# Kernel tuning notes

Measured on AMD Instinct MI355X. Metric: run time of the kernel, lower is better.

## Reference

```python
import jax, jax.numpy as jnp
import numpy as np

BATCH = 4096
FEATURES = 64
VOCAB = 580000
EMB_DIM = 32
MODELS = 512
SEQ_LEN = 128


def _positional_encoding(position, d_model):
    # Faithful to the numpy get_angles: 1/10000^(2*(i//2)/d_model), sin on even, cos on odd.
    pos = jnp.arange(position, dtype=jnp.float32)[:, None]          # [P, 1]
    i = jnp.arange(d_model, dtype=jnp.float32)[None, :]             # [1, D]
    angle_rates = 1.0 / jnp.power(10000.0, (2.0 * jnp.floor(i / 2.0)) / jnp.float32(d_model))
    angles = pos * angle_rates                                      # [P, D]
    even = (jnp.arange(d_model) % 2 == 0)[None, :]
    pe = jnp.where(even, jnp.sin(angles), jnp.cos(angles))
    return pe[None]                                                 # [1, P, D]


def setup_inputs() -> dict:
    key = jax.random.key(0)
    k1, k2, k3 = jax.random.split(key, 3)
    tokens = jax.random.randint(k1, (BATCH, FEATURES), 0, VOCAB, dtype=jnp.int32)
    emb_table = jax.random.normal(k2, (VOCAB, EMB_DIM), dtype=jnp.float32)
    W = jax.random.normal(k3, (FEATURES * EMB_DIM, MODELS), dtype=jnp.float32) * 0.02
    b = jnp.zeros((MODELS,), dtype=jnp.float32)
    return {"tokens": tokens, "emb_table": emb_table, "W": W, "b": b}


def reference(tokens, emb_table, W, b):
    B, F = tokens.shape
    # gather + scale by sqrt(models)
    x = emb_table[tokens] * jnp.sqrt(jnp.float32(MODELS))           # [B, F, E]
    x = x.reshape(B, F * EMB_DIM)                                   # [B, F*E]
    x = x @ W + b                                                   # [B, M]
    # tf.tile(row, [seq_len]) then reshape (seq_len, models) == broadcast over seq axis
    pe = _positional_encoding(SEQ_LEN, MODELS)                      # [1, S, M]
    out = x[:, None, :] + pe[:, :SEQ_LEN, :]                        # [B, S, M]
    return out
```

## Files before the change

### kernel.cpp

```cpp
#include <hip/hip_runtime.h>
#include <math.h>

#define BATCH   4096
#define FEAT    64
#define EMB     32
#define MODELS  512
#define SEQ     128
#define KDIM    (FEAT * EMB)

#define SQRT_MODELS 22.62741699796952f
#define LN10000     9.210340371976184f

typedef __attribute__((ext_vector_type(4))) float        f32x4;
typedef __attribute__((ext_vector_type(8))) short        bf16x8;
typedef __attribute__((ext_vector_type(4))) unsigned int u32x4;

#define WT_BYTES  ((size_t)MODELS * KDIM * 2)
#define PE_BYTES  ((size_t)SEQ * MODELS * 4)
#define X_BYTES   ((size_t)BATCH * MODELS * 4)
#define ABF_BYTES ((size_t)BATCH * KDIM * 2)
#define WS_MID    (WT_BYTES + PE_BYTES + X_BYTES)
#define WS_FULL   (WT_BYTES + PE_BYTES + X_BYTES + ABF_BYTES)

__device__ inline unsigned short bf16_rne(float f) {
    unsigned int b = __builtin_bit_cast(unsigned int, f);
    return (unsigned short)((b + 0x7FFFu + ((b >> 16) & 1u)) >> 16);
}

#define CVT_PK4(pk, v0, v1)                                                     \
    {                                                                           \
        unsigned int q0, q1, q2, q3;                                            \
        asm("v_cvt_pk_bf16_f32 %0, %1, %2" : "=v"(q0) : "v"(v0.x), "v"(v0.y));  \
        asm("v_cvt_pk_bf16_f32 %0, %1, %2" : "=v"(q1) : "v"(v0.z), "v"(v0.w));  \
        asm("v_cvt_pk_bf16_f32 %0, %1, %2" : "=v"(q2) : "v"(v1.x), "v"(v1.y));  \
        asm("v_cvt_pk_bf16_f32 %0, %1, %2" : "=v"(q3) : "v"(v1.z), "v"(v1.w));  \
        pk = (u32x4){q0, q1, q2, q3};                                           \
    }

__global__ __launch_bounds__(256)
void prep_all(const int* __restrict__ tokens, const float* __restrict__ emb,
              const float* __restrict__ W, const float* __restrict__ bias,
              unsigned short* __restrict__ Wt, float* __restrict__ pe,
              unsigned short* __restrict__ Abf) {
    const int bx  = blockIdx.x;
    const int tid = threadIdx.x;

    if (bx < 1024) {
        __shared__ float t[32][33];
        const int k0 = (bx & 63) * 32;
        const int n0 = (bx >> 6) * 32;
        const int tx = tid & 31;
        const int ty = tid >> 5;
        #pragma unroll
        for (int i = 0; i < 4; ++i)
            t[ty + i * 8][tx] = W[(size_t)(k0 + ty + i * 8) * MODELS + n0 + tx] * SQRT_MODELS;
        __syncthreads();
        #pragma unroll
        for (int i = 0; i < 4; ++i)
            Wt[(size_t)(n0 + ty + i * 8) * KDIM + k0 + tx] = bf16_rne(t[tx][ty + i * 8]);
    } else if (bx < 1280) {
        const int idx = (bx - 1024) * 256 + tid;
        const int s = idx >> 9;
        const int m = idx & (MODELS - 1);
        const float rate = expf(-LN10000 * (float)(2 * (m >> 1)) * (1.0f / 512.0f));
        const float ang  = (float)s * rate;
        pe[idx] = ((m & 1) ? cosf(ang) : sinf(ang)) + bias[m];
    } else {
        const int g    = (bx - 1280) * 256 + tid;
        const int fr   = g >> 2;
        const int part = g & 3;
        const int tok  = tokens[fr];
        const float* src = emb + (size_t)tok * EMB + part * 8;
        const f32x4 v0 = *(const f32x4*)src;
        const f32x4 v1 = *(const f32x4*)(src + 4);
        u32x4 pk;
        CVT_PK4(pk, v0, v1);
        *(u32x4*)(Abf + (size_t)g * 8) = pk;
    }
}

__global__ __launch_bounds__(256)
void gemm_dense(const unsigned short* __restrict__ Abf,
                const unsigned short* __restrict__ Wt,
                float* __restrict__ x) {
    const int tid  = threadIdx.x;
    const int lane = tid & 63;
    const int wave = tid >> 6;
    const int ln   = lane & 15;
    const int kg   = lane >> 4;
    const int m0 = blockIdx.x * 64 + (wave >> 1) * 32;
    const int n0 = blockIdx.y * 64 + (wave & 1) * 32;

    const unsigned short* a0p = Abf + (size_t)(m0 + ln) * KDIM + kg * 8;
    const unsigned short* a1p = a0p + 16 * KDIM;
    const unsigned short* b0p = Wt + (size_t)(n0 + ln) * KDIM + kg * 8;
    const unsigned short* b1p = b0p + 16 * KDIM;

    f32x4 acc00 = {0,0,0,0}, acc01 = {0,0,0,0};
    f32x4 acc10 = {0,0,0,0}, acc11 = {0,0,0,0};

    #pragma unroll 8
    for (int k = 0; k < KDIM; k += 32) {
        const bf16x8 a0 = *(const bf16x8*)(a0p + k);
        const bf16x8 a1 = *(const bf16x8*)(a1p + k);
        const bf16x8 b0 = *(const bf16x8*)(b0p + k);
        const bf16x8 b1 = *(const bf16x8*)(b1p + k);
        acc00 = __builtin_amdgcn_mfma_f32_16x16x32_bf16(a0, b0, acc00, 0, 0, 0);
        acc01 = __builtin_amdgcn_mfma_f32_16x16x32_bf16(a0, b1, acc01, 0, 0, 0);
        acc10 = __builtin_amdgcn_mfma_f32_16x16x32_bf16(a1, b0, acc10, 0, 0, 0);
        acc11 = __builtin_amdgcn_mfma_f32_16x16x32_bf16(a1, b1, acc11, 0, 0, 0);
    }
    #pragma unroll
    for (int q = 0; q < 4; ++q) {
        const int r = kg * 4 + q;
        x[(size_t)(m0 + r)      * MODELS + n0 + ln]      = acc00[q];
        x[(size_t)(m0 + r)      * MODELS + n0 + 16 + ln] = acc01[q];
        x[(size_t)(m0 + 16 + r) * MODELS + n0 + ln]      = acc10[q];
        x[(size_t)(m0 + 16 + r) * MODELS + n0 + 16 + ln] = acc11[q];
    }
}

__global__ __launch_bounds__(256)
void bcast_pe(const float* __restrict__ x, const float* __restrict__ pe,
              float* __restrict__ out) {
    const int tid = threadIdx.x;
    const int m4  = tid & 127;
    const int b   = blockIdx.x * 2 + (tid >> 7);
    const f32x4 xv = *(const f32x4*)(x + (size_t)b * MODELS + m4 * 4);
    const f32x4* pev = (const f32x4*)pe;
    float* ob = out + (size_t)b * SEQ * MODELS + m4 * 4;
    #pragma unroll 16
    for (int s = 0; s < SEQ; ++s) {
        const f32x4 p = pev[s * 128 + m4];
        __builtin_nontemporal_store(xv + p, (f32x4*)(ob + (size_t)s * MODELS));
    }
}

__global__ __launch_bounds__(256)
void gemm_mfma(const int* __restrict__ tokens, const float* __restrict__ emb,
               const unsigned short* __restrict__ Wt, float* __restrict__ x) {
    const int tid  = threadIdx.x;
    const int wave = tid >> 6;
    const int lane = tid & 63;
    const int ln   = lane & 15;
    const int kg   = lane >> 4;
    const int m_base = blockIdx.y * 16;
    const int n_base = blockIdx.x * 256 + wave * 64;
    const int* trow = tokens + (size_t)(m_base + ln) * FEAT;
    const unsigned short* bptr[4];
    #pragma unroll
    for (int nf = 0; nf < 4; ++nf)
        bptr[nf] = Wt + (size_t)(n_base + nf * 16 + ln) * KDIM + kg * 8;
    f32x4 acc[4] = {f32x4{0,0,0,0}, f32x4{0,0,0,0}, f32x4{0,0,0,0}, f32x4{0,0,0,0}};
    for (int f4 = 0; f4 < FEAT; f4 += 4) {
        const int4 tok4 = *(const int4*)(trow + f4);
        const int toks[4] = {tok4.x, tok4.y, tok4.z, tok4.w};
        #pragma unroll
        for (int j = 0; j < 4; ++j) {
            const int f = f4 + j;
            const float* ea = emb + (size_t)toks[j] * EMB + kg * 8;
            const f32x4 a0 = *(const f32x4*)ea;
            const f32x4 a1 = *(const f32x4*)(ea + 4);
            u32x4 pk;
            CVT_PK4(pk, a0, a1);
            const bf16x8 afrag = __builtin_bit_cast(bf16x8, pk);
            #pragma unroll
            for (int nf = 0; nf < 4; ++nf) {
                const bf16x8 bfrag = *(const bf16x8*)(bptr[nf] + (size_t)f * EMB);
                acc[nf] = __builtin_amdgcn_mfma_f32_16x16x32_bf16(afrag, bfrag, acc[nf], 0, 0, 0);
            }
        }
    }
    #pragma unroll
    for (int nf = 0; nf < 4; ++nf)
        #pragma unroll
        for (int q = 0; q < 4; ++q)
            x[(size_t)(m_base + kg * 4 + q) * MODELS + n_base + nf * 16 + ln] = acc[nf][q];
}

__global__ __launch_bounds__(256)
void prep_wt(const float* __restrict__ W, unsigned short* __restrict__ Wt) {
    __shared__ float t[32][33];
    const int k0 = blockIdx.x * 32;
    const int n0 = blockIdx.y * 32;
    const int tx = threadIdx.x;
    const int ty = threadIdx.y;
    #pragma unroll
    for (int i = 0; i < 4; ++i)
        t[ty + i * 8][tx] = W[(size_t)(k0 + ty + i * 8) * MODELS + n0 + tx] * SQRT_MODELS;
    __syncthreads();
    #pragma unroll
    for (int i = 0; i < 4; ++i)
        Wt[(size_t)(n0 + ty + i * 8) * KDIM + k0 + tx] = bf16_rne(t[tx][ty + i * 8]);
}

__global__ __launch_bounds__(256)
void prep_pe(const float* __restrict__ bias, float* __restrict__ pe) {
    const int idx = blockIdx.x * 256 + threadIdx.x;
    const int s = idx >> 9;
    const int m = idx & (MODELS - 1);
    const float rate = expf(-LN10000 * (float)(2 * (m >> 1)) * (1.0f / 512.0f));
    const float ang  = (float)s * rate;
    pe[idx] = ((m & 1) ? cosf(ang) : sinf(ang)) + bias[m];
}

#define BM 64
#define BN 64
#define BK 32
__global__ __launch_bounds__(256, 2)
void fused_emb_gemm_pe(const int* __restrict__ tokens, const float* __restrict__ emb,
                       const float* __restrict__ W, const float* __restrict__ bias,
                       float* __restrict__ out) {
    __shared__ float As[BK][BM];
    __shared__ float Bs[BK][BN];
    __shared__ float peS[SEQ][BN];
    const int tid  = threadIdx.x;
    const int bn   = blockIdx.x * BN;
    const int brow = blockIdx.y * BM;
    for (int idx = tid; idx < SEQ * BN; idx += 256) {
        const int s  = idx >> 6;
        const int ml = idx & 63;
        const int m  = bn + ml;
        const float rate = expf(-LN10000 * (float)(2 * (m >> 1)) * (1.0f / 512.0f));
        const float ang  = (float)s * rate;
        peS[s][ml] = (m & 1) ? cosf(ang) : sinf(ang);
    }
    float acc[4][4] = {};
    const int tx = tid & 15;
    const int ty = tid >> 4;
    const int lr = tid >> 2;
    const int lj = tid & 3;
    const int bk = tid >> 4;
    const int bc = (tid & 15) * 4;
    for (int kt = 0; kt < FEAT; ++kt) {
        __syncthreads();
        {
            const int tok = tokens[(brow + lr) * FEAT + kt];
            const float* erow = emb + (size_t)tok * EMB + lj * 8;
            const float4 a0 = *(const float4*)(erow);
            const float4 a1 = *(const float4*)(erow + 4);
            const int k0 = lj * 8;
            As[k0 + 0][lr] = a0.x * SQRT_MODELS; As[k0 + 1][lr] = a0.y * SQRT_MODELS;
            As[k0 + 2][lr] = a0.z * SQRT_MODELS; As[k0 + 3][lr] = a0.w * SQRT_MODELS;
            As[k0 + 4][lr] = a1.x * SQRT_MODELS; As[k0 + 5][lr] = a1.y * SQRT_MODELS;
            As[k0 + 6][lr] = a1.z * SQRT_MODELS; As[k0 + 7][lr] = a1.w * SQRT_MODELS;
        }
        {
            const float* w0 = W + (size_t)(kt * 32 + bk) * MODELS + bn + bc;
            const float* w1 = W + (size_t)(kt * 32 + bk + 16) * MODELS + bn + bc;
            *(float4*)&Bs[bk][bc]      = *(const float4*)w0;
            *(float4*)&Bs[bk + 16][bc] = *(const float4*)w1;
        }
        __syncthreads();
        #pragma unroll
        for (int k = 0; k < BK; ++k) {
            const float4 a = *(const float4*)&As[k][ty * 4];
            const float4 b = *(const float4*)&Bs[k][tx * 4];
            acc[0][0] += a.x * b.x; acc[0][1] += a.x * b.y; acc[0][2] += a.x * b.z; acc[0][3] += a.x * b.w;
            acc[1][0] += a.y * b.x; acc[1][1] += a.y * b.y; acc[1][2] += a.y * b.z; acc[1][3] += a.y * b.w;
            acc[2][0] += a.z * b.x; acc[2][1] += a.z * b.y; acc[2][2] += a.z * b.z; acc[2][3] += a.z * b.w;
            acc[3][0] += a.w * b.x; acc[3][1] += a.w * b.y; acc[3][2] += a.w * b.z; acc[3][3] += a.w * b.w;
        }
    }
    {
        const float4 bv = *(const float4*)(bias + bn + tx * 4);
        #pragma unroll
        for (int i = 0; i < 4; ++i) {
            acc[i][0] += bv.x; acc[i][1] += bv.y; acc[i][2] += bv.z; acc[i][3] += bv.w;
        }
    }
    size_t rowbase[4];
    #pragma unroll
    for (int i = 0; i < 4; ++i)
        rowbase[i] = ((size_t)(brow + ty * 4 + i) * SEQ) * MODELS + bn + tx * 4;
    #pragma unroll 4
    for (int s = 0; s < SEQ; ++s) {
        const float4 pv = *(const float4*)&peS[s][tx * 4];
        const size_t soff = (size_t)s * MODELS;
        #pragma unroll
        for (int i = 0; i < 4; ++i) {
            float4 o;
            o.x = acc[i][0] + pv.x; o.y = acc[i][1] + pv.y;
            o.z = acc[i][2] + pv.z; o.w = acc[i][3] + pv.w;
            *(float4*)(out + rowbase[i] + soff) = o;
        }
    }
}

extern "C" void kernel_launch(void* const* d_in, const int* in_sizes, int n_in,
                              void* d_out, int out_size, void* d_ws, size_t ws_size,
                              hipStream_t stream) {
    const int*   tokens = (const int*)d_in[0];
    const float* emb    = (const float*)d_in[1];
    const float* W      = (const float*)d_in[2];
    const float* bias   = (const float*)d_in[3];
    float*       out    = (float*)d_out;

    if (ws_size >= WS_FULL) {
        char* w = (char*)d_ws;
        unsigned short* Wt  = (unsigned short*)w;
        float*          pe  = (float*)(w + WT_BYTES);
        float*          x   = (float*)(w + WT_BYTES + PE_BYTES);
        unsigned short* Abf = (unsigned short*)(w + WT_BYTES + PE_BYTES + X_BYTES);

        prep_all<<<dim3(1024 + 256 + 4096), dim3(256), 0, stream>>>(
            tokens, emb, W, bias, Wt, pe, Abf);
        gemm_dense<<<dim3(BATCH / 64, MODELS / 64), dim3(256), 0, stream>>>(Abf, Wt, x);
        bcast_pe<<<dim3(BATCH / 2), dim3(256), 0, stream>>>(x, pe, out);
    } else if (ws_size >= WS_MID) {
        char* w = (char*)d_ws;
        unsigned short* Wt = (unsigned short*)w;
        float* pe = (float*)(w + WT_BYTES);
        float* x  = (float*)(w + WT_BYTES + PE_BYTES);

        prep_wt<<<dim3(KDIM / 32, MODELS / 32), dim3(32, 8), 0, stream>>>(W, Wt);
        prep_pe<<<dim3(SEQ * MODELS / 256), dim3(256), 0, stream>>>(bias, pe);
        gemm_mfma<<<dim3(MODELS / 256, BATCH / 16), dim3(256), 0, stream>>>(tokens, emb, Wt, x);
        bcast_pe<<<dim3(BATCH / 2), dim3(256), 0, stream>>>(x, pe, out);
    } else {
        fused_emb_gemm_pe<<<dim3(MODELS / BN, BATCH / BM), dim3(256), 0, stream>>>(
            tokens, emb, W, bias, out);
    }
}
```

Before: 268.5 us.

## Split GEMM K dimension across two wave groups with LDS reduction

The dense bf16 MFMA GEMM now launches 512-thread blocks. Two groups of four waves each compute half of the K range for the same 64x64 output tile, and the partial sums are reduced through a shared-memory buffer before the store. This doubles the waves in flight per tile to hide global-load latency in a loop that reads operands directly from global memory. It adds a barrier, LDS traffic and about 16KB of shared memory per block.

```diff
diff --git a/kernel.cpp b/kernel.cpp
--- a/kernel.cpp
+++ b/kernel.cpp
@@ -79,28 +79,36 @@
     }
 }
 
-__global__ __launch_bounds__(256)
-void gemm_dense(const unsigned short* __restrict__ Abf,
-                const unsigned short* __restrict__ Wt,
-                float* __restrict__ x) {
+__global__ __launch_bounds__(512)
+void gemm_ksplit(const unsigned short* __restrict__ Abf,
+                 const unsigned short* __restrict__ Wt,
+                 float* __restrict__ x) {
+    __shared__ float red[64][65];
+
     const int tid  = threadIdx.x;
     const int lane = tid & 63;
     const int wave = tid >> 6;
     const int ln   = lane & 15;
     const int kg   = lane >> 4;
-    const int m0 = blockIdx.x * 64 + (wave >> 1) * 32;
-    const int n0 = blockIdx.y * 64 + (wave & 1) * 32;
-
-    const unsigned short* a0p = Abf + (size_t)(m0 + ln) * KDIM + kg * 8;
+    const int qd   = wave & 3;
+    const int kh   = wave >> 2;
+
+    const int br = (qd >> 1) * 32;
+    const int bc = (qd & 1) * 32;
+    const int m0 = blockIdx.x * 64 + br;
+    const int n0 = blockIdx.y * 64 + bc;
+    const int k0 = kh * (KDIM / 2);
+
+    const unsigned short* a0p = Abf + (size_t)(m0 + ln) * KDIM + k0 + kg * 8;
     const unsigned short* a1p = a0p + 16 * KDIM;
-    const unsigned short* b0p = Wt + (size_t)(n0 + ln) * KDIM + kg * 8;
+    const unsigned short* b0p = Wt + (size_t)(n0 + ln) * KDIM + k0 + kg * 8;
     const unsigned short* b1p = b0p + 16 * KDIM;
 
     f32x4 acc00 = {0,0,0,0}, acc01 = {0,0,0,0};
     f32x4 acc10 = {0,0,0,0}, acc11 = {0,0,0,0};
 
-    #pragma unroll 8
-    for (int k = 0; k < KDIM; k += 32) {
+    #pragma unroll 4
+    for (int k = 0; k < KDIM / 2; k += 32) {
         const bf16x8 a0 = *(const bf16x8*)(a0p + k);
         const bf16x8 a1 = *(const bf16x8*)(a1p + k);
         const bf16x8 b0 = *(const bf16x8*)(b0p + k);
@@ -110,13 +118,27 @@
         acc10 = __builtin_amdgcn_mfma_f32_16x16x32_bf16(a1, b0, acc10, 0, 0, 0);
         acc11 = __builtin_amdgcn_mfma_f32_16x16x32_bf16(a1, b1, acc11, 0, 0, 0);
     }
-    #pragma unroll
-    for (int q = 0; q < 4; ++q) {
-        const int r = kg * 4 + q;
-        x[(size_t)(m0 + r)      * MODELS + n0 + ln]      = acc00[q];
-        x[(size_t)(m0 + r)      * MODELS + n0 + 16 + ln] = acc01[q];
-        x[(size_t)(m0 + 16 + r) * MODELS + n0 + ln]      = acc10[q];
-        x[(size_t)(m0 + 16 + r) * MODELS + n0 + 16 + ln] = acc11[q];
+
+    if (kh == 1) {
+        #pragma unroll
+        for (int q = 0; q < 4; ++q) {
+            const int r = kg * 4 + q;
+            red[br + r][bc + ln]           = acc00[q];
+            red[br + r][bc + 16 + ln]      = acc01[q];
+            red[br + 16 + r][bc + ln]      = acc10[q];
+            red[br + 16 + r][bc + 16 + ln] = acc11[q];
+        }
+    }
+    __syncthreads();
+    if (kh == 0) {
+        #pragma unroll
+        for (int q = 0; q < 4; ++q) {
+            const int r = kg * 4 + q;
+            x[(size_t)(m0 + r)      * MODELS + n0 + ln]      = acc00[q] + red[br + r][bc + ln];
+            x[(size_t)(m0 + r)      * MODELS + n0 + 16 + ln] = acc01[q] + red[br + r][bc + 16 + ln];
+            x[(size_t)(m0 + 16 + r) * MODELS + n0 + ln]      = acc10[q] + red[br + 16 + r][bc + ln];
+            x[(size_t)(m0 + 16 + r) * MODELS + n0 + 16 + ln] = acc11[q] + red[br + 16 + r][bc + 16 + ln];
+        }
     }
 }
 
@@ -305,7 +327,7 @@
 
         prep_all<<<dim3(1024 + 256 + 4096), dim3(256), 0, stream>>>(
             tokens, emb, W, bias, Wt, pe, Abf);
-        gemm_dense<<<dim3(BATCH / 64, MODELS / 64), dim3(256), 0, stream>>>(Abf, Wt, x);
+        gemm_ksplit<<<dim3(BATCH / 64, MODELS / 64), dim3(512), 0, stream>>>(Abf, Wt, x);
         bcast_pe<<<dim3(BATCH / 2), dim3(256), 0, stream>>>(x, pe, out);
     } else if (ws_size >= WS_MID) {
         char* w = (char*)d_ws;
```

Result: no change. 269.4 us (+0.4%).
